# Performance work log

Hardware: AMD Instinct MI355X
Metric: run time of the kernel (lower is better)

Reference implementation:

```python
import jax, jax.numpy as jnp
import numpy as np

HQ, HK, DH = 32, 8, 64
ROPE_BASE = 10000.0


def _rope_tables(T, dtype):
    pos = jnp.arange(T, dtype=jnp.float32)
    inv_freq = 1.0 / (ROPE_BASE ** (jnp.arange(0, DH, 2, dtype=jnp.float32) / DH))
    freqs = pos[:, None] * inv_freq[None, :]          # (T, DH/2)
    cos = jnp.concatenate([jnp.cos(freqs), jnp.cos(freqs)], -1).astype(dtype)  # (T, DH)
    sin = jnp.concatenate([jnp.sin(freqs), jnp.sin(freqs)], -1).astype(dtype)
    return cos, sin


def _rotate_half(t):
    return jnp.concatenate([-t[..., DH // 2:], t[..., :DH // 2]], -1)


def setup_inputs() -> dict:
    key = jax.random.key(0)
    k1, k2, k3, k4 = jax.random.split(key, 4)
    B, T, D = 2, 2048, 2048
    std = 0.02 / np.sqrt(24)
    kv_std = std / np.sqrt(HQ / HK)
    return {
        "x": jax.random.normal(k1, (B, T, D), jnp.float32),
        "Wq": jax.random.normal(k2, (D, HQ * DH), jnp.float32) * std,
        "Wkv": jax.random.normal(k3, (D, 2 * HK * DH), jnp.float32) * kv_std,
        "Wo": jax.random.normal(k4, (HQ * DH, D), jnp.float32) * std,
    }


def reference(x, Wq, Wkv, Wo):
    B, T, D = x.shape
    g = HQ // HK
    scale = DH ** -0.5
    # projections
    q = (x @ Wq).reshape(B, T, HQ, DH).transpose(0, 2, 1, 3)       # (B,Hq,T,Dh)
    kv = (x @ Wkv).reshape(B, T, 2, HK, DH)
    k = kv[:, :, 0].transpose(0, 2, 1, 3)                           # (B,Hk,T,Dh)
    v = kv[:, :, 1].transpose(0, 2, 1, 3)
    # GQA expand: each kv head repeated g times consecutively
    k = jnp.repeat(k, g, axis=1)                                    # (B,Hq,T,Dh)
    v = jnp.repeat(v, g, axis=1)
    # RoPE on q and repeated k
    cos, sin = _rope_tables(T, x.dtype)
    q = q * cos + _rotate_half(q) * sin
    k = k * cos + _rotate_half(k) * sin
    # attention
    scores = jnp.einsum('bhqd,bhkd->bhqk', q, k) * scale            # (B,Hq,T,T)
    causal = jnp.triu(jnp.ones((T, T), bool), 1)
    scores = jnp.where(causal, -jnp.inf, scores)
    attn = jax.nn.softmax(scores.astype(jnp.float32), axis=-1).astype(x.dtype)
    out = jnp.einsum('bhqk,bhkd->bhqd', attn, v)                    # (B,Hq,T,Dh)
    out = out.transpose(0, 2, 1, 3).reshape(B, T, HQ * DH)
    return out @ Wo
```

## Files before the change

kernel.cpp:

```cpp
#include <hip/hip_runtime.h>
#include <hip/hip_bf16.h>

#define DEVI __device__ __forceinline__

typedef __attribute__((ext_vector_type(4))) float f32x4;
typedef __attribute__((ext_vector_type(16))) float f32x16;
typedef __attribute__((ext_vector_type(8))) short s16x8;
typedef __attribute__((ext_vector_type(4))) short s16x4;
typedef __attribute__((ext_vector_type(2))) unsigned u32x2;

DEVI ushort f2bf(float f) {
  union { float f; unsigned u; } v; v.f = f;
  unsigned r = v.u + 0x7FFFu + ((v.u >> 16) & 1u);
  return (ushort)(r >> 16);
}

DEVI void gload_lds16(const void* g, void* l) {
  __builtin_amdgcn_global_load_lds((const __attribute__((address_space(1))) void*)g,
                                   (__attribute__((address_space(3))) void*)l, 16, 0, 0);
}

#define MFMA16 __builtin_amdgcn_mfma_f32_16x16x32_bf16
#define MFMA32 __builtin_amdgcn_mfma_f32_32x32x16_bf16
#define SBAR() __builtin_amdgcn_s_barrier()
#define LGKM0() asm volatile("s_waitcnt lgkmcnt(0)")

DEVI float plswap_max(float x) {
  union { float f; unsigned u; } a; a.f = x;
  u32x2 r = __builtin_amdgcn_permlane32_swap(a.u, a.u, false, false);
  union { unsigned u; float f; } o0, o1; o0.u = r[0]; o1.u = r[1];
  return fmaxf(o0.f, o1.f);
}
DEVI float plswap_sum(float x) {
  union { float f; unsigned u; } a; a.f = x;
  u32x2 r = __builtin_amdgcn_permlane32_swap(a.u, a.u, false, false);
  union { unsigned u; float f; } o0, o1; o0.u = r[0]; o1.u = r[1];
  return o0.f + o1.f;
}

DEVI void stage128q(const ushort* __restrict__ gsrc, int K, ushort* ld, int tid) {
  #pragma unroll
  for (int j = 0; j < 4; ++j) {
    const int ci = j * 256 + tid;
    const int row = ci >> 3, c = ci & 7;
    gload_lds16(gsrc + (size_t)row * K + ((c ^ (row & 7)) << 3),
                ld + (size_t)(j * 256 + (tid & ~63)) * 8);
  }
}
DEVI s16x8 ldfrag(const ushort* tile, int row, int kc) {
  return *(const s16x8*)((const char*)tile + row * 128 + ((kc ^ (row & 7)) << 4));
}

DEVI void kloop3(const ushort* __restrict__ A, const ushort* __restrict__ BT,
                 ushort* Asm, ushort* Bsm, int m0, int n0, int K, int NKT,
                 f32x4 (&acc)[4][4], int tid, int wm, int wn, int g, int l15) {
  stage128q(A + (size_t)m0 * K, K, Asm, tid);
  stage128q(BT + (size_t)n0 * K, K, Bsm, tid);
  stage128q(BT + (size_t)n0 * K + 64, K, Bsm + 8192, tid);
  asm volatile("s_waitcnt vmcnt(4)");
  SBAR();

  int rd = 0;
  #pragma unroll 1
  for (int t = 0; t < NKT; ++t) {
    const ushort* Ah = Asm + (t & 1) * 8192;
    const ushort* Bh = Bsm + rd * 8192;
    s16x8 af[4][2], bfr[4][2];

    #pragma unroll
    for (int ks = 0; ks < 2; ++ks) {
      #pragma unroll
      for (int ni = 0; ni < 4; ++ni)
        bfr[ni][ks] = ldfrag(Bh, wn * 64 + ni * 16 + l15, ks * 4 + g);
      #pragma unroll
      for (int mi = 0; mi < 4; ++mi)
        af[mi][ks] = ldfrag(Ah, wm * 64 + mi * 16 + l15, ks * 4 + g);
    }
    if (t + 1 < NKT)
      stage128q(A + (size_t)m0 * K + (t + 1) * 64, K, Asm + ((t + 1) & 1) * 8192, tid);
    int wr = rd + 2; if (wr >= 3) wr -= 3;
    if (t + 2 < NKT)
      stage128q(BT + (size_t)n0 * K + (t + 2) * 64, K, Bsm + wr * 8192, tid);

    LGKM0();
    __builtin_amdgcn_sched_barrier(0);
    __builtin_amdgcn_s_setprio(1);
    #pragma unroll
    for (int mi = 0; mi < 4; ++mi)
      #pragma unroll
      for (int ni = 0; ni < 2; ++ni)
        #pragma unroll
        for (int ks = 0; ks < 2; ++ks)
          acc[mi][ni] = MFMA16(af[mi][ks], bfr[ni][ks], acc[mi][ni], 0, 0, 0);
    #pragma unroll
    for (int mi = 0; mi < 4; ++mi)
      #pragma unroll
      for (int ni = 0; ni < 2; ++ni)
        #pragma unroll
        for (int ks = 0; ks < 2; ++ks)
          acc[mi][2 + ni] = MFMA16(af[mi][ks], bfr[2 + ni][ks], acc[mi][2 + ni], 0, 0, 0);
    __builtin_amdgcn_s_setprio(0);

    if (t + 2 < NKT)      asm volatile("s_waitcnt vmcnt(4)");
    else if (t + 1 < NKT) asm volatile("s_waitcnt vmcnt(0)");
    SBAR();
    rd = (rd == 2) ? 0 : rd + 1;
  }
}

__global__ __launch_bounds__(256) void preamble_k(const float* __restrict__ x,
                                                  const float* __restrict__ Wq,
                                                  const float* __restrict__ Wkv,
                                                  const float* __restrict__ Wo,
                                                  ushort* __restrict__ xb,
                                                  ushort* __restrict__ WqkvT,
                                                  ushort* __restrict__ WoT,
                                                  float2* __restrict__ tab) {
  const int id = blockIdx.x;
  const int tid = threadIdx.x;

  if (id >= 2560) {
    if (id < 10752) {
      const int lid = id - 2560;
      int i = (lid * 256 + tid) * 4;
      float4 v = *(const float4*)(x + i);
      ushort4 o;
      o.x = f2bf(v.x); o.y = f2bf(v.y); o.z = f2bf(v.z); o.w = f2bf(v.w);
      *(ushort4*)(xb + i) = o;
    } else {
      const int lid = id - 10752;
      int idx = lid * 256 + tid;
      int t = idx >> 5, i = idx & 31;
      float inv = expf(-(float)i * 0.28782313662425575f);
      float ang = (float)t * inv;
      tab[idx] = make_float2(cosf(ang), sinf(ang));
    }
    return;
  }

  __shared__ ushort tile[64][66];
  const float* in; ushort* out; int R, C, bx, by;
  if (id < 1024)        { in = Wq;  out = WqkvT;              R = 2048; C = 2048; bx = id & 31;          by = id >> 5; }
  else if (id < 1536)   { in = Wkv; out = WqkvT + 2048*2048;  R = 2048; C = 1024; bx = (id-1024) & 15;   by = (id-1024) >> 4; }
  else                  { in = Wo;  out = WoT;                R = 2048; C = 2048; bx = (id-1536) & 31;   by = (id-1536) >> 5; }
  const int r0 = by * 64, c0 = bx * 64;
  #pragma unroll
  for (int j = 0; j < 16; ++j) {
    int idx = j * 256 + tid;
    int r = idx >> 6, c = idx & 63;
    tile[c][r] = f2bf(in[(size_t)(r0 + r) * C + c0 + c]);
  }
  __syncthreads();
  #pragma unroll
  for (int j = 0; j < 16; ++j) {
    int idx = j * 256 + tid;
    int c = idx >> 6, r = idx & 63;
    out[(size_t)(c0 + c) * R + r0 + r] = tile[c][r];
  }
}

__global__ __launch_bounds__(256) void gemm_qkv_3b(const ushort* __restrict__ A,
                                                   const ushort* __restrict__ BT,
                                                   const float2* __restrict__ tab,
                                                   ushort* __restrict__ Qp,
                                                   ushort* __restrict__ Kp,
                                                   ushort* __restrict__ Vp) {
  constexpr int K = 2048, NKT = 32;
  __shared__ __attribute__((aligned(128))) ushort smem[40960];
  ushort* Asm = smem;
  ushort* Bsm = smem + 16384;
  ushort* Ot = smem;

  const int tid = threadIdx.x;
  const int ln = tid & 63, wv = tid >> 6;
  const int g = ln >> 4, l15 = ln & 15, l31 = ln & 31, hi = ln >> 5;
  const int wm = wv >> 1, wn = wv & 1;
  const int m0 = blockIdx.y * 128, n0 = blockIdx.x * 128;

  f32x4 acc[4][4];
  #pragma unroll
  for (int i = 0; i < 4; ++i)
    #pragma unroll
    for (int j = 0; j < 4; ++j) acc[i][j] = (f32x4){0.f, 0.f, 0.f, 0.f};

  kloop3(A, BT, Asm, Bsm, m0, n0, K, NKT, acc, tid, wm, wn, g, l15);

  __syncthreads();
  const int bq = m0 >> 11;
  const int tg0 = m0 & 2047;
  const int type = (n0 < 2048) ? 0 : (n0 < 2560 ? 1 : 2);

  #pragma unroll
  for (int mi = 0; mi < 4; ++mi)
    #pragma unroll
    for (int r = 0; r < 4; ++r) {
      const int tl = wm * 64 + mi * 16 + g * 4 + r;
      const int t = tg0 + tl;
      #pragma unroll
      for (int ni = 0; ni < 4; ++ni) {
        const int cl = wn * 64 + ni * 16 + l15;
        float val = acc[mi][ni][r];
        float outv;
        if (type < 2) {
          float pairv = acc[mi][ni ^ 2][r];
          float2 cs = tab[t * 32 + (ni & 1) * 16 + l15];
          outv = (ni & 2) ? (val * cs.x + pairv * cs.y) : (val * cs.x - pairv * cs.y);
          if (type == 0) outv *= 0.18033688011112042f;
        } else {
          outv = val;
        }
        Ot[tl * 132 + cl] = f2bf(outv);
      }
    }
  __syncthreads();

  #pragma unroll
  for (int it = 0; it < 8; ++it) {
    const int id = wv * 8 + it;
    const int hl = id >> 4, q4 = (id >> 2) & 3, fi = id & 3;
    const int tile = (tg0 >> 5) + q4;
    if (type < 2) {
      const ushort* srow = Ot + (q4 * 32 + l31) * 132 + hl * 64 + fi * 16 + hi * 8;
      union { s16x4 h[2]; s16x8 v; } u;
      u.h[0] = *(const s16x4*)srow;
      u.h[1] = *(const s16x4*)(srow + 4);
      ushort* dst;
      if (type == 0) {
        const int h = (n0 >> 6) + hl;
        dst = Qp + (((size_t)(bq * 32 + h) * 64 + tile) * 4 + fi) * 512 + ln * 8;
      } else {
        const int h = ((n0 - 2048) >> 6) + hl;
        dst = Kp + (((size_t)(bq * 8 + h) * 64 + tile) * 4 + fi) * 512 + ln * 8;
      }
      *(s16x8*)dst = u.v;
    } else {
      const int hk = ((n0 - 2560) >> 6) + hl;
      const int col = hl * 64 + (fi & 1) * 32 + l31;
      const int row0 = q4 * 32 + (fi >> 1) * 16 + hi * 8;
      ushort o[8];
      #pragma unroll
      for (int j = 0; j < 8; ++j) o[j] = Ot[(row0 + j) * 132 + col];
      ushort* dst = Vp + (((size_t)(bq * 8 + hk) * 64 + tile) * 4 + fi) * 512 + ln * 8;
      *(s16x8*)dst = *(const s16x8*)o;
    }
  }
}

__global__ __launch_bounds__(256) void gemm_bt_3b(const ushort* __restrict__ A,
                                                  const ushort* __restrict__ BT,
                                                  float* __restrict__ C, int M, int N, int K) {
  __shared__ __attribute__((aligned(128))) ushort smem[40960];
  ushort* Asm = smem;
  ushort* Bsm = smem + 16384;

  const int tid = threadIdx.x;
  const int ln = tid & 63, wv = tid >> 6;
  const int g = ln >> 4, l15 = ln & 15;
  const int wm = wv >> 1, wn = wv & 1;
  const int m0 = blockIdx.y * 128, n0 = blockIdx.x * 128;
  const int NKT = K / 64;

  f32x4 acc[4][4];
  #pragma unroll
  for (int i = 0; i < 4; ++i)
    #pragma unroll
    for (int j = 0; j < 4; ++j) acc[i][j] = (f32x4){0.f, 0.f, 0.f, 0.f};

  kloop3(A, BT, Asm, Bsm, m0, n0, K, NKT, acc, tid, wm, wn, g, l15);

  #pragma unroll
  for (int mi = 0; mi < 4; ++mi)
    #pragma unroll
    for (int r = 0; r < 4; ++r) {
      int row = m0 + wm * 64 + mi * 16 + g * 4 + r;
      float* crow = C + (size_t)row * N + n0 + wn * 64 + l15;
      #pragma unroll
      for (int ni = 0; ni < 4; ++ni) crow[ni * 16] = acc[mi][ni][r];
    }
}

__global__ __attribute__((amdgpu_flat_work_group_size(64, 64)))
__attribute__((amdgpu_waves_per_eu(2, 2)))
void attn_k(const ushort* __restrict__ Qp,
            const ushort* __restrict__ Kp,
            const ushort* __restrict__ Vp,
            ushort* __restrict__ O) {
  __shared__ ushort ep[2][32 * 64];
  const int ln = threadIdx.x & 63;
  const int l31 = ln & 31, hi = ln >> 5;

  const int f = blockIdx.x;
  const int xcd = f & 7, j = f >> 3;
  const int pr = xcd + 8 * (j & 1);
  const int b = pr >> 3, hk = pr & 7;
  const int s = j >> 1;
  const int hp = s & 1;
  const int hq0 = hk * 4 + hp * 2, hq1 = hq0 + 1;
  const int qtile = 63 - (s >> 1);
  const int qw = qtile * 32;
  const int nt = qtile + 1;

  const ushort* QhA   = Qp + ((size_t)(b * 32 + hq0)) * (64 * 2048);
  const ushort* QhB   = Qp + ((size_t)(b * 32 + hq1)) * (64 * 2048);
  const ushort* Kbase = Kp + ((size_t)(b * 8 + hk)) * (64 * 2048);
  const ushort* Vbase = Vp + ((size_t)(b * 8 + hk)) * (64 * 2048);

  s16x8 qfA[4], qfB[4];
  {
    const ushort* qa = QhA + (size_t)qtile * 2048 + ln * 8;
    const ushort* qb = QhB + (size_t)qtile * 2048 + ln * 8;
    #pragma unroll
    for (int ks = 0; ks < 4; ++ks) {
      qfA[ks] = *(const s16x8*)(qa + ks * 512);
      qfB[ks] = *(const s16x8*)(qb + ks * 512);
    }
  }

  f32x16 z16;
  #pragma unroll
  for (int r = 0; r < 16; ++r) z16[r] = 0.f;

  f32x16 oaccA[2], oaccB[2];
  #pragma unroll
  for (int r = 0; r < 16; ++r) {
    oaccA[0][r] = 0.f; oaccA[1][r] = 0.f;
    oaccB[0][r] = 0.f; oaccB[1][r] = 0.f;
  }
  float mA = -1e30f, lA = 0.f, mB = -1e30f, lB = 0.f;

  const ushort* kp = Kbase + ln * 8;
  const ushort* vp = Vbase + ln * 8;

  s16x8 kf[4];
  #pragma unroll
  for (int ks = 0; ks < 4; ++ks) kf[ks] = *(const s16x8*)(kp + ks * 512);
  kp += 2048;

  s16x8 vc[4];
  union pfu { unsigned u[4]; s16x8 v; };
  pfu pfA0, pfA1, pfB0, pfB1;

  #pragma unroll 1
  for (int kt = 0; kt < nt; ++kt) {
    if (kt) {
      __builtin_amdgcn_s_setprio(1);
      oaccA[0] = MFMA32(vc[0], pfA0.v, oaccA[0], 0, 0, 0);
      oaccB[0] = MFMA32(vc[0], pfB0.v, oaccB[0], 0, 0, 0);
      oaccA[1] = MFMA32(vc[1], pfA0.v, oaccA[1], 0, 0, 0);
      oaccB[1] = MFMA32(vc[1], pfB0.v, oaccB[1], 0, 0, 0);
      oaccA[0] = MFMA32(vc[2], pfA1.v, oaccA[0], 0, 0, 0);
      oaccB[0] = MFMA32(vc[2], pfB1.v, oaccB[0], 0, 0, 0);
      oaccA[1] = MFMA32(vc[3], pfA1.v, oaccA[1], 0, 0, 0);
      oaccB[1] = MFMA32(vc[3], pfB1.v, oaccB[1], 0, 0, 0);
      __builtin_amdgcn_s_setprio(0);
    }
    #pragma unroll
    for (int fi2 = 0; fi2 < 4; ++fi2) vc[fi2] = *(const s16x8*)(vp + fi2 * 512);
    vp += 2048;

    __builtin_amdgcn_s_setprio(1);
    f32x16 spA = MFMA32(kf[0], qfA[0], z16, 0, 0, 0);
    f32x16 spB = MFMA32(kf[0], qfB[0], z16, 0, 0, 0);
    spA = MFMA32(kf[1], qfA[1], spA, 0, 0, 0);
    spB = MFMA32(kf[1], qfB[1], spB, 0, 0, 0);
    spA = MFMA32(kf[2], qfA[2], spA, 0, 0, 0);
    spB = MFMA32(kf[2], qfB[2], spB, 0, 0, 0);
    spA = MFMA32(kf[3], qfA[3], spA, 0, 0, 0);
    spB = MFMA32(kf[3], qfB[3], spB, 0, 0, 0);
    __builtin_amdgcn_s_setprio(0);

    if (kt + 1 < nt) {
      #pragma unroll
      for (int ks = 0; ks < 4; ++ks) kf[ks] = *(const s16x8*)(kp + ks * 512);
      kp += 2048;
    }

    if (kt == qtile) {
      #pragma unroll
      for (int r = 0; r < 16; ++r) {
        int key = (r & 3) + 8 * (r >> 2) + 4 * hi;
        if (key > l31) { spA[r] = -1e30f; spB[r] = -1e30f; }
      }
    }

    float pa, pb;
    {
      float t0 = fmaxf(fmaxf(spA[0], spA[1]), spA[2]);
      float t1 = fmaxf(fmaxf(spA[3], spA[4]), spA[5]);
      float t2 = fmaxf(fmaxf(spA[6], spA[7]), spA[8]);
      float t3 = fmaxf(fmaxf(spA[9], spA[10]), spA[11]);
      float t4 = fmaxf(fmaxf(spA[12], spA[13]), spA[14]);
      pa = plswap_max(fmaxf(fmaxf(fmaxf(t0, t1), t2), fmaxf(fmaxf(t3, t4), spA[15])));
      float u0 = fmaxf(fmaxf(spB[0], spB[1]), spB[2]);
      float u1 = fmaxf(fmaxf(spB[3], spB[4]), spB[5]);
      float u2 = fmaxf(fmaxf(spB[6], spB[7]), spB[8]);
      float u3 = fmaxf(fmaxf(spB[9], spB[10]), spB[11]);
      float u4 = fmaxf(fmaxf(spB[12], spB[13]), spB[14]);
      pb = plswap_max(fmaxf(fmaxf(fmaxf(u0, u1), u2), fmaxf(fmaxf(u3, u4), spB[15])));
    }

    if (__any(pa - mA > 8.0f)) {
      float mn = fmaxf(mA, pa);
      float alpha = __builtin_amdgcn_exp2f(mA - mn);
      mA = mn; lA *= alpha;
      #pragma unroll
      for (int r = 0; r < 16; ++r) { oaccA[0][r] *= alpha; oaccA[1][r] *= alpha; }
    }
    if (__any(pb - mB > 8.0f)) {
      float mn = fmaxf(mB, pb);
      float alpha = __builtin_amdgcn_exp2f(mB - mn);
      mB = mn; lB *= alpha;
      #pragma unroll
      for (int r = 0; r < 16; ++r) { oaccB[0][r] *= alpha; oaccB[1][r] *= alpha; }
    }

    #pragma unroll
    for (int r = 0; r < 16; ++r) {
      spA[r] = __builtin_amdgcn_exp2f(spA[r] - mA);
      spB[r] = __builtin_amdgcn_exp2f(spB[r] - mB);
    }
    {
      float a0 = spA[0] + spA[1], a1 = spA[2] + spA[3], a2 = spA[4] + spA[5], a3 = spA[6] + spA[7];
      float a4 = spA[8] + spA[9], a5 = spA[10] + spA[11], a6 = spA[12] + spA[13], a7 = spA[14] + spA[15];
      lA += plswap_sum(((a0 + a1) + (a2 + a3)) + ((a4 + a5) + (a6 + a7)));
      float b0 = spB[0] + spB[1], b1 = spB[2] + spB[3], b2 = spB[4] + spB[5], b3 = spB[6] + spB[7];
      float b4 = spB[8] + spB[9], b5 = spB[10] + spB[11], b6 = spB[12] + spB[13], b7 = spB[14] + spB[15];
      lB += plswap_sum(((b0 + b1) + (b2 + b3)) + ((b4 + b5) + (b6 + b7)));
    }

    unsigned cwA[8], cwB[8];
    #pragma unroll
    for (int jj = 0; jj < 8; ++jj) {
      union { __hip_bfloat162 h; unsigned u; } pk;
      pk.h = __float22bfloat162_rn(make_float2(spA[2 * jj], spA[2 * jj + 1]));
      cwA[jj] = pk.u;
      pk.h = __float22bfloat162_rn(make_float2(spB[2 * jj], spB[2 * jj + 1]));
      cwB[jj] = pk.u;
    }
    {
      u32x2 r;
      r = __builtin_amdgcn_permlane32_swap(cwA[0], cwA[2], false, false);
      pfA0.u[0] = r[0]; pfA0.u[2] = r[1];
      r = __builtin_amdgcn_permlane32_swap(cwA[1], cwA[3], false, false);
      pfA0.u[1] = r[0]; pfA0.u[3] = r[1];
      r = __builtin_amdgcn_permlane32_swap(cwA[4], cwA[6], false, false);
      pfA1.u[0] = r[0]; pfA1.u[2] = r[1];
      r = __builtin_amdgcn_permlane32_swap(cwA[5], cwA[7], false, false);
      pfA1.u[1] = r[0]; pfA1.u[3] = r[1];
      r = __builtin_amdgcn_permlane32_swap(cwB[0], cwB[2], false, false);
      pfB0.u[0] = r[0]; pfB0.u[2] = r[1];
      r = __builtin_amdgcn_permlane32_swap(cwB[1], cwB[3], false, false);
      pfB0.u[1] = r[0]; pfB0.u[3] = r[1];
      r = __builtin_amdgcn_permlane32_swap(cwB[4], cwB[6], false, false);
      pfB1.u[0] = r[0]; pfB1.u[2] = r[1];
      r = __builtin_amdgcn_permlane32_swap(cwB[5], cwB[7], false, false);
      pfB1.u[1] = r[0]; pfB1.u[3] = r[1];
    }
  }

  __builtin_amdgcn_s_setprio(1);
  oaccA[0] = MFMA32(vc[0], pfA0.v, oaccA[0], 0, 0, 0);
  oaccB[0] = MFMA32(vc[0], pfB0.v, oaccB[0], 0, 0, 0);
  oaccA[1] = MFMA32(vc[1], pfA0.v, oaccA[1], 0, 0, 0);
  oaccB[1] = MFMA32(vc[1], pfB0.v, oaccB[1], 0, 0, 0);
  oaccA[0] = MFMA32(vc[2], pfA1.v, oaccA[0], 0, 0, 0);
  oaccB[0] = MFMA32(vc[2], pfB1.v, oaccB[0], 0, 0, 0);
  oaccA[1] = MFMA32(vc[3], pfA1.v, oaccA[1], 0, 0, 0);
  oaccB[1] = MFMA32(vc[3], pfB1.v, oaccB[1], 0, 0, 0);
  __builtin_amdgcn_s_setprio(0);

  const int qr = ln >> 1, half = ln & 1;
  {
    float invl = 1.0f / lA;
    ushort* lds = ep[0];
    #pragma unroll
    for (int dt = 0; dt < 2; ++dt)
      #pragma unroll
      for (int r = 0; r < 16; ++r) {
        int d = dt * 32 + (r & 3) + 8 * (r >> 2) + 4 * hi;
        int byte = (l31 * 128 + d * 2) ^ ((l31 & 7) << 4);
        *(ushort*)((char*)lds + byte) = f2bf(oaccA[dt][r] * invl);
      }
    #pragma unroll
    for (int jj = 0; jj < 4; ++jj) {
      int byte = (qr * 128 + half * 64 + jj * 16) ^ ((qr & 7) << 4);
      s16x8 vrow = *(const s16x8*)((const char*)lds + byte);
      *(s16x8*)(O + ((size_t)(b * 2048 + qw + qr)) * 2048 + hq0 * 64 + half * 32 + jj * 8) = vrow;
    }
  }
  {
    float invl = 1.0f / lB;
    ushort* lds = ep[1];
    #pragma unroll
    for (int dt = 0; dt < 2; ++dt)
      #pragma unroll
      for (int r = 0; r < 16; ++r) {
        int d = dt * 32 + (r & 3) + 8 * (r >> 2) + 4 * hi;
        int byte = (l31 * 128 + d * 2) ^ ((l31 & 7) << 4);
        *(ushort*)((char*)lds + byte) = f2bf(oaccB[dt][r] * invl);
      }
    #pragma unroll
    for (int jj = 0; jj < 4; ++jj) {
      int byte = (qr * 128 + half * 64 + jj * 16) ^ ((qr & 7) << 4);
      s16x8 vrow = *(const s16x8*)((const char*)lds + byte);
      *(s16x8*)(O + ((size_t)(b * 2048 + qw + qr)) * 2048 + hq1 * 64 + half * 32 + jj * 8) = vrow;
    }
  }
}

extern "C" void kernel_launch(void* const* d_in, const int* in_sizes, int n_in,
                              void* d_out, int out_size, void* d_ws, size_t ws_size,
                              hipStream_t stream) {
  const float* x   = (const float*)d_in[0];
  const float* Wq  = (const float*)d_in[1];
  const float* Wkv = (const float*)d_in[2];
  const float* Wo  = (const float*)d_in[3];
  float* out = (float*)d_out;

  char* ws = (char*)d_ws;
  ushort* xb     = (ushort*)(ws);
  ushort* WqkvT  = (ushort*)(ws + 16777216);
  ushort* WoT    = (ushort*)(ws + 29360128);
  float2* tab    = (float2*)(ws + 37748736);
  ushort* Qp     = (ushort*)(ws + 38273024);
  ushort* Kp     = (ushort*)(ws + 55050240);
  ushort* Vp     = (ushort*)(ws + 59244544);
  ushort* Ob     = (ushort*)(ws + 63438848);

  preamble_k<<<11008, 256, 0, stream>>>(x, Wq, Wkv, Wo, xb, WqkvT, WoT, tab);
  gemm_qkv_3b<<<dim3(24, 32), 256, 0, stream>>>(xb, WqkvT, tab, Qp, Kp, Vp);
  attn_k<<<2048, 64, 0, stream>>>(Qp, Kp, Vp, Ob);
  gemm_bt_3b<<<dim3(16, 32), 256, 0, stream>>>(Ob, WoT, out, 4096, 2048, 2048);
}
```

Before: 200.9 us.

## Pre-pack x into MFMA fragment layout and load A fragments directly from global

```diff
diff --git a/kernel.cpp b/kernel.cpp
--- a/kernel.cpp
+++ b/kernel.cpp
@@ -112,7 +112,7 @@
                                                   const float* __restrict__ Wq,
                                                   const float* __restrict__ Wkv,
                                                   const float* __restrict__ Wo,
-                                                  ushort* __restrict__ xb,
+                                                  ushort* __restrict__ Apack,
                                                   ushort* __restrict__ WqkvT,
                                                   ushort* __restrict__ WoT,
                                                   float2* __restrict__ tab) {
@@ -120,15 +120,24 @@
   const int tid = threadIdx.x;
 
   if (id >= 2560) {
-    if (id < 10752) {
+    if (id < 4608) {
       const int lid = id - 2560;
-      int i = (lid * 256 + tid) * 4;
-      float4 v = *(const float4*)(x + i);
-      ushort4 o;
-      o.x = f2bf(v.x); o.y = f2bf(v.y); o.z = f2bf(v.z); o.w = f2bf(v.w);
-      *(ushort4*)(xb + i) = o;
+      const int rb = lid >> 5, t = lid & 31;
+      const int mi = tid >> 6, ln = tid & 63;
+      const int l15 = ln & 15, g = ln >> 4;
+      const float* src = x + (size_t)(rb * 64 + mi * 16 + l15) * 2048 + t * 64 + g * 8;
+      ushort* dst = Apack + ((size_t)((rb * 32 + t) * 4 + mi) * 2) * 512 + ln * 8;
+      #pragma unroll
+      for (int ks = 0; ks < 2; ++ks) {
+        float4 v0 = *(const float4*)(src + ks * 32);
+        float4 v1 = *(const float4*)(src + ks * 32 + 4);
+        ushort o[8];
+        o[0] = f2bf(v0.x); o[1] = f2bf(v0.y); o[2] = f2bf(v0.z); o[3] = f2bf(v0.w);
+        o[4] = f2bf(v1.x); o[5] = f2bf(v1.y); o[6] = f2bf(v1.z); o[7] = f2bf(v1.w);
+        *(s16x8*)(dst + ks * 512) = *(const s16x8*)o;
+      }
     } else {
-      const int lid = id - 10752;
+      const int lid = id - 4608;
       int idx = lid * 256 + tid;
       int t = idx >> 5, i = idx & 31;
       float inv = expf(-(float)i * 0.28782313662425575f);
@@ -159,16 +168,15 @@
   }
 }
 
-__global__ __launch_bounds__(256) void gemm_qkv_3b(const ushort* __restrict__ A,
+__global__ __launch_bounds__(256) void gemm_qkv_ap(const ushort* __restrict__ Apack,
                                                    const ushort* __restrict__ BT,
                                                    const float2* __restrict__ tab,
                                                    ushort* __restrict__ Qp,
                                                    ushort* __restrict__ Kp,
                                                    ushort* __restrict__ Vp) {
   constexpr int K = 2048, NKT = 32;
-  __shared__ __attribute__((aligned(128))) ushort smem[40960];
-  ushort* Asm = smem;
-  ushort* Bsm = smem + 16384;
+  __shared__ __attribute__((aligned(128))) ushort smem[24576];
+  ushort* Bsm = smem;
   ushort* Ot = smem;
 
   const int tid = threadIdx.x;
@@ -177,13 +185,70 @@
   const int wm = wv >> 1, wn = wv & 1;
   const int m0 = blockIdx.y * 128, n0 = blockIdx.x * 128;
 
+  const ushort* apw = Apack + (size_t)((m0 >> 6) + wm) * 32 * 4096 + ln * 8;
+
   f32x4 acc[4][4];
   #pragma unroll
   for (int i = 0; i < 4; ++i)
     #pragma unroll
     for (int j = 0; j < 4; ++j) acc[i][j] = (f32x4){0.f, 0.f, 0.f, 0.f};
 
-  kloop3(A, BT, Asm, Bsm, m0, n0, K, NKT, acc, tid, wm, wn, g, l15);
+  s16x8 afA[4][2], afB[4][2];
+
+#define LOADAF(DST, T)                                                        \
+  {                                                                           \
+    const ushort* p_ = apw + (size_t)(T) * 4096;                              \
+    _Pragma("unroll")                                                         \
+    for (int mi_ = 0; mi_ < 4; ++mi_)                                         \
+      _Pragma("unroll")                                                       \
+      for (int ks_ = 0; ks_ < 2; ++ks_)                                       \
+        DST[mi_][ks_] = *(const s16x8*)(p_ + (mi_ * 2 + ks_) * 512);          \
+  }
+
+  LOADAF(afA, 0);
+  stage128q(BT + (size_t)n0 * K, K, Bsm, tid);
+  stage128q(BT + (size_t)n0 * K + 64, K, Bsm + 8192, tid);
+  asm volatile("s_waitcnt vmcnt(4)");
+  SBAR();
+
+#define SUBITER(U, AFCUR, AFNXT)                                              \
+  {                                                                           \
+    const int u_ = (U);                                                       \
+    if (u_ + 1 < NKT) LOADAF(AFNXT, u_ + 1);                                  \
+    int wr_ = (u_ + 2) % 3;                                                   \
+    if (u_ + 2 < NKT)                                                         \
+      stage128q(BT + (size_t)n0 * K + (u_ + 2) * 64, K, Bsm + wr_ * 8192, tid);\
+    const ushort* Bh_ = Bsm + (u_ % 3) * 8192;                                \
+    s16x8 bfr_[4][2];                                                         \
+    _Pragma("unroll")                                                         \
+    for (int ks_ = 0; ks_ < 2; ++ks_)                                         \
+      _Pragma("unroll")                                                       \
+      for (int ni_ = 0; ni_ < 4; ++ni_)                                       \
+        bfr_[ni_][ks_] = ldfrag(Bh_, wn * 64 + ni_ * 16 + l15, ks_ * 4 + g);  \
+    LGKM0();                                                                  \
+    __builtin_amdgcn_sched_barrier(0);                                        \
+    __builtin_amdgcn_s_setprio(1);                                            \
+    _Pragma("unroll")                                                         \
+    for (int mi_ = 0; mi_ < 4; ++mi_)                                         \
+      _Pragma("unroll")                                                       \
+      for (int ni_ = 0; ni_ < 4; ++ni_)                                       \
+        _Pragma("unroll")                                                     \
+        for (int ks_ = 0; ks_ < 2; ++ks_)                                     \
+          acc[mi_][ni_] = MFMA16(AFCUR[mi_][ks_], bfr_[ni_][ks_],             \
+                                 acc[mi_][ni_], 0, 0, 0);                     \
+    __builtin_amdgcn_s_setprio(0);                                            \
+    if (u_ + 2 < NKT)      asm volatile("s_waitcnt vmcnt(4)");                \
+    else if (u_ + 1 < NKT) asm volatile("s_waitcnt vmcnt(0)");                \
+    SBAR();                                                                   \
+  }
+
+  #pragma unroll 1
+  for (int t = 0; t < NKT; t += 2) {
+    SUBITER(t,     afA, afB);
+    SUBITER(t + 1, afB, afA);
+  }
+#undef SUBITER
+#undef LOADAF
 
   __syncthreads();
   const int bq = m0 >> 11;
@@ -518,7 +583,7 @@
   float* out = (float*)d_out;
 
   char* ws = (char*)d_ws;
-  ushort* xb     = (ushort*)(ws);
+  ushort* Apack  = (ushort*)(ws);
   ushort* WqkvT  = (ushort*)(ws + 16777216);
   ushort* WoT    = (ushort*)(ws + 29360128);
   float2* tab    = (float2*)(ws + 37748736);
@@ -527,8 +592,8 @@
   ushort* Vp     = (ushort*)(ws + 59244544);
   ushort* Ob     = (ushort*)(ws + 63438848);
 
-  preamble_k<<<11008, 256, 0, stream>>>(x, Wq, Wkv, Wo, xb, WqkvT, WoT, tab);
-  gemm_qkv_3b<<<dim3(24, 32), 256, 0, stream>>>(xb, WqkvT, tab, Qp, Kp, Vp);
+  preamble_k<<<4864, 256, 0, stream>>>(x, Wq, Wkv, Wo, Apack, WqkvT, WoT, tab);
+  gemm_qkv_ap<<<dim3(24, 32), 256, 0, stream>>>(Apack, WqkvT, tab, Qp, Kp, Vp);
   attn_k<<<2048, 64, 0, stream>>>(Qp, Kp, Vp, Ob);
   gemm_bt_3b<<<dim3(16, 32), 256, 0, stream>>>(Ob, WoT, out, 4096, 2048, 2048);
 }
```

Result: slower. 215.4 us (+7.2%).
